# Kernel optimization log

Measured on AMD Instinct MI355X. Metric: run time of the kernel, lower is better.

The kernel has to match this reference:

```python
import jax, jax.numpy as jnp
import numpy as np

B, N, VDIM = 64, 256, 2048
LRDIM, EMBED = 64, 1024


def setup_inputs() -> dict:
    key = jax.random.key(0)
    ks = jax.random.split(key, 12)
    s = 1.0 / np.sqrt(VDIM)
    return {
        "Vmat": jax.random.normal(ks[0], (B, N, VDIM), dtype=jnp.float32),
        # weight-normed linear_U1: W = g * v / ||v||_row, bias b
        "U1_v": jax.random.normal(ks[1], (LRDIM, VDIM), dtype=jnp.float32) * s,
        "U1_g": jax.random.uniform(ks[2], (LRDIM,), dtype=jnp.float32, minval=0.5, maxval=1.5),
        "U1_b": jax.random.normal(ks[3], (LRDIM,), dtype=jnp.float32) * s,
        "U2_v": jax.random.normal(ks[4], (LRDIM, VDIM), dtype=jnp.float32) * s,
        "U2_g": jax.random.uniform(ks[5], (LRDIM,), dtype=jnp.float32, minval=0.5, maxval=1.5),
        "U2_b": jax.random.normal(ks[6], (LRDIM,), dtype=jnp.float32) * s,
        # final projection + BatchNorm1d affine params
        "W_lin": jax.random.normal(ks[7], (EMBED, VDIM), dtype=jnp.float32) * s,
        "b_lin": jax.random.normal(ks[8], (EMBED,), dtype=jnp.float32) * s,
        "bn_gamma": jnp.ones((EMBED,), dtype=jnp.float32),
        "bn_beta": jnp.zeros((EMBED,), dtype=jnp.float32),
    }


def _weight_norm(v, g):
    # torch weight_norm with dim=0: per output row
    return v * (g / jnp.linalg.norm(v, axis=1))[:, None]


def reference(Vmat, U1_v, U1_g, U1_b, U2_v, U2_g, U2_b, W_lin, b_lin, bn_gamma, bn_beta):
    # forward(Vmat, t_method='uncorr', model_num=6) -> UnCorrVmat_Detail path
    W1 = _weight_norm(U1_v, U1_g)
    W2 = _weight_norm(U2_v, U2_g)
    right = jax.nn.relu(jnp.einsum('bnv,kv->bnk', Vmat, W1) + U1_b)   # [B,N,LR]
    left = jax.nn.relu(jnp.einsum('bnv,kv->bnk', Vmat, W2) + U2_b)    # [B,N,LR]
    uncorr = jnp.einsum('bnk,bmk->bnm', left, right)                   # [B,N,N]
    # vectorized per-batch diag rsqrt normalization
    d = jax.lax.rsqrt(jnp.einsum('bii->bi', uncorr) + 1e-6)            # [B,N]
    uncorr = d[:, None, :] * uncorr * d[:, :, None]
    uncorr = 1.0 + jnp.eye(Vmat.shape[1], dtype=Vmat.dtype) - uncorr
    feats = jnp.mean(jnp.einsum('bnm,bmv->bnv', uncorr, Vmat), axis=1)  # [B,VDIM]
    # linear + BatchNorm1d (training mode: biased batch stats)
    x = feats @ W_lin.T + b_lin                                        # [B,EMBED]
    mu = jnp.mean(x, axis=0)
    var = jnp.mean(jnp.square(x - mu), axis=0)
    return bn_gamma * (x - mu) * jax.lax.rsqrt(var + 1e-5) + bn_beta
```

## Files before the change

### kernel.cpp

```cpp
#include <hip/hip_runtime.h>

#define B_ 64
#define N_ 256
#define V_ 2048
#define E_ 1024
#define MROWS 16384

typedef __bf16 bf16_t;
typedef bf16_t bf16x8 __attribute__((ext_vector_type(8)));
typedef float f32x4 __attribute__((ext_vector_type(4)));

#define OFF_S   0
#define OFF_LR  16384
#define OFF_FT  2113536
#define FTSZ    131072
#define OFF_WB  2637824

__device__ __forceinline__ void gload_lds16(const bf16_t* g, bf16_t* l) {
    __builtin_amdgcn_global_load_lds((const __attribute__((address_space(1))) void*)g,
                                     (__attribute__((address_space(3))) void*)l, 16, 0, 0);
}

__global__ void kprep(const float* __restrict__ U1v, const float* __restrict__ U1g,
                      const float* __restrict__ U2v, const float* __restrict__ U2g,
                      bf16_t* __restrict__ Wb) {
    __shared__ float red[256];
    __shared__ float sc;
    const int r = blockIdx.x;
    const float* v = (r < 64) ? (U1v + (size_t)r * V_) : (U2v + (size_t)(r - 64) * V_);
    float ss = 0.f;
    for (int i = threadIdx.x; i < V_; i += 256) { float x = v[i]; ss += x * x; }
    red[threadIdx.x] = ss;
    __syncthreads();
    for (int o = 128; o > 0; o >>= 1) {
        if (threadIdx.x < (unsigned)o) red[threadIdx.x] += red[threadIdx.x + o];
        __syncthreads();
    }
    if (threadIdx.x == 0) {
        float g = (r < 64) ? U1g[r] : U2g[r - 64];
        sc = g * rsqrtf(red[0]);
    }
    __syncthreads();
    const float s = sc;
    const int k = threadIdx.x * 8;
    float4 f0 = *(const float4*)(v + k);
    float4 f1 = *(const float4*)(v + k + 4);
    bf16x8 o;
    o[0] = (bf16_t)(f0.x * s); o[1] = (bf16_t)(f0.y * s);
    o[2] = (bf16_t)(f0.z * s); o[3] = (bf16_t)(f0.w * s);
    o[4] = (bf16_t)(f1.x * s); o[5] = (bf16_t)(f1.y * s);
    o[6] = (bf16_t)(f1.z * s); o[7] = (bf16_t)(f1.w * s);
    *(bf16x8*)(Wb + (size_t)r * V_ + k) = o;
}

#define BK 128
__global__ __launch_bounds__(256) void gemm_lr(
    const float* __restrict__ V, const bf16_t* __restrict__ Wb,
    const float* __restrict__ U1b, const float* __restrict__ U2b,
    float* __restrict__ LR) {
    __shared__ bf16_t As[32 * BK];
    __shared__ bf16_t Bs[128 * BK];
    const int t = threadIdx.x;
    const int m0 = blockIdx.x * 32;
    const int wv = t >> 6, lane = t & 63;
    const int lm = lane & 15, lq = lane >> 4;
    const int n0w = wv * 32;

    const int ar = t >> 3, au = t & 7;
    const float* aptr = V + (size_t)(m0 + ar) * V_ + au * 8;
    bf16_t* adst0 = &As[ar * BK + ((au ^ (ar & 15)) * 8)];
    bf16_t* adst1 = &As[ar * BK + (((au + 8) ^ (ar & 15)) * 8)];

    const int rloc = lane >> 4, cc = lane & 15;
    const int r15 = wv * 4 + rloc;
    const bf16_t* bgsrc = Wb + (size_t)r15 * V_ + (cc ^ r15) * 8;

    f32x4 acc[2][2];
#pragma unroll
    for (int i = 0; i < 2; ++i)
#pragma unroll
        for (int j = 0; j < 2; ++j) acc[i][j] = (f32x4){0.f, 0.f, 0.f, 0.f};

#pragma unroll
    for (int q = 0; q < 8; ++q)
        gload_lds16(bgsrc + (size_t)q * 16 * V_, &Bs[(q * 16 + wv * 4) * BK]);
    float4 ap0 = *(const float4*)(aptr);
    float4 ap1 = *(const float4*)(aptr + 4);
    float4 ap2 = *(const float4*)(aptr + 64);
    float4 ap3 = *(const float4*)(aptr + 68);

    for (int k0 = 0; k0 < V_; k0 += BK) {
        bf16x8 av0, av1;
        av0[0] = (bf16_t)ap0.x; av0[1] = (bf16_t)ap0.y; av0[2] = (bf16_t)ap0.z; av0[3] = (bf16_t)ap0.w;
        av0[4] = (bf16_t)ap1.x; av0[5] = (bf16_t)ap1.y; av0[6] = (bf16_t)ap1.z; av0[7] = (bf16_t)ap1.w;
        av1[0] = (bf16_t)ap2.x; av1[1] = (bf16_t)ap2.y; av1[2] = (bf16_t)ap2.z; av1[3] = (bf16_t)ap2.w;
        av1[4] = (bf16_t)ap3.x; av1[5] = (bf16_t)ap3.y; av1[6] = (bf16_t)ap3.z; av1[7] = (bf16_t)ap3.w;
        *(bf16x8*)adst0 = av0;
        *(bf16x8*)adst1 = av1;
        __syncthreads();

#pragma unroll
        for (int h = 0; h < 2; ++h) {
            bf16x8 af[2][2], bfr[2][2];
#pragma unroll
            for (int i = 0; i < 2; ++i)
#pragma unroll
                for (int kf = 0; kf < 2; ++kf)
                    af[i][kf] = *(bf16x8*)&As[(i * 16 + lm) * BK + ((((h * 2 + kf) * 4 + lq) ^ lm) * 8)];
#pragma unroll
            for (int j = 0; j < 2; ++j)
#pragma unroll
                for (int kf = 0; kf < 2; ++kf)
                    bfr[j][kf] = *(bf16x8*)&Bs[(n0w + j * 16 + lm) * BK + ((((h * 2 + kf) * 4 + lq) ^ lm) * 8)];
            if (h == 1 && k0 + BK < V_) {
                ap0 = *(const float4*)(aptr + k0 + BK);
                ap1 = *(const float4*)(aptr + k0 + BK + 4);
                ap2 = *(const float4*)(aptr + k0 + BK + 64);
                ap3 = *(const float4*)(aptr + k0 + BK + 68);
            }
#pragma unroll
            for (int i = 0; i < 2; ++i)
#pragma unroll
                for (int j = 0; j < 2; ++j) {
                    acc[i][j] = __builtin_amdgcn_mfma_f32_16x16x32_bf16(af[i][0], bfr[j][0], acc[i][j], 0, 0, 0);
                    acc[i][j] = __builtin_amdgcn_mfma_f32_16x16x32_bf16(af[i][1], bfr[j][1], acc[i][j], 0, 0, 0);
                }
        }
        __syncthreads();
        if (k0 + BK < V_) {
#pragma unroll
            for (int q = 0; q < 8; ++q)
                gload_lds16(bgsrc + (size_t)q * 16 * V_ + (k0 + BK), &Bs[(q * 16 + wv * 4) * BK]);
        }
    }
#pragma unroll
    for (int j = 0; j < 2; ++j) {
        const int n = n0w + j * 16 + lm;
        const float bi = (n < 64) ? U1b[n] : U2b[n - 64];
#pragma unroll
        for (int i = 0; i < 2; ++i)
#pragma unroll
            for (int r = 0; r < 4; ++r) {
                const int m = m0 + i * 16 + lq * 4 + r;
                LR[(size_t)m * 128 + n] = fmaxf(acc[i][j][r] + bi, 0.f);
            }
    }
}

__global__ __launch_bounds__(256) void kds(const float* __restrict__ LR, float* __restrict__ s) {
    __shared__ float dl[256];
    __shared__ float red[4][64];
    __shared__ float lbar[64];
    const int b = blockIdx.x, t = threadIdx.x;
    const float* Lb = LR + (size_t)b * N_ * 128;
    const float* row = Lb + (size_t)t * 128;
    float dd = 0.f;
#pragma unroll
    for (int k = 0; k < 64; k += 4) {
        float4 l = *(const float4*)(row + k);
        float4 r = *(const float4*)(row + 64 + k);
        dd += l.x * r.x + l.y * r.y + l.z * r.z + l.w * r.w;
    }
    const float dv = rsqrtf(dd + 1e-6f);
    dl[t] = dv;
    __syncthreads();
    const int k = t & 63, g = t >> 6;
    float acc = 0.f;
    for (int n = g; n < N_; n += 4)
        acc += dl[n] * Lb[(size_t)n * 128 + 64 + k];
    red[g][k] = acc;
    __syncthreads();
    if (t < 64) lbar[t] = red[0][t] + red[1][t] + red[2][t] + red[3][t];
    __syncthreads();
    float a2 = 0.f;
#pragma unroll 8
    for (int kk = 0; kk < 64; ++kk) a2 += lbar[kk] * row[kk];
    s[b * N_ + t] = ((float)(N_ + 1) - dv * a2) * (1.0f / (float)N_);
}

__global__ __launch_bounds__(256) void kfeats(const float* __restrict__ Vmat,
                                              const float* __restrict__ s,
                                              float* __restrict__ ftp) {
    const int b = blockIdx.x >> 3, vc = (blockIdx.x >> 2) & 1, mc = blockIdx.x & 3;
    __shared__ float sl[64];
    const int t = threadIdx.x;
    if (t < 64) sl[t] = s[b * N_ + mc * 64 + t];
    __syncthreads();
    const int v = vc * 1024 + t * 4;
    const float* base = Vmat + (size_t)b * N_ * V_ + (size_t)mc * 64 * V_ + v;
    float4 a = {0.f, 0.f, 0.f, 0.f};
    for (int m = 0; m < 64; m += 16) {
        float4 x[16];
#pragma unroll
        for (int u = 0; u < 16; ++u) x[u] = *(const float4*)(base + (size_t)(m + u) * V_);
#pragma unroll
        for (int u = 0; u < 16; ++u) {
            float sv = sl[m + u];
            a.x += sv * x[u].x; a.y += sv * x[u].y;
            a.z += sv * x[u].z; a.w += sv * x[u].w;
        }
    }
    float* dst = ftp + (size_t)mc * FTSZ;
    dst[(size_t)(v + 0) * 64 + b] = a.x;
    dst[(size_t)(v + 1) * 64 + b] = a.y;
    dst[(size_t)(v + 2) * 64 + b] = a.z;
    dst[(size_t)(v + 3) * 64 + b] = a.w;
}

__global__ __launch_bounds__(512) void klinbn(const float* __restrict__ ftp,
                                              const float* __restrict__ Wl,
                                              const float* __restrict__ gamma,
                                              const float* __restrict__ beta,
                                              float* __restrict__ out) {
    __shared__ float red[8][4][64];
    const int e0 = blockIdx.x * 4;
    const int t = threadIdx.x, b = t & 63, g = t >> 6;
    const float* w0 = Wl + (size_t)(e0 + 0) * V_ + g * 256;
    const float* w1 = Wl + (size_t)(e0 + 1) * V_ + g * 256;
    const float* w2 = Wl + (size_t)(e0 + 2) * V_ + g * 256;
    const float* w3 = Wl + (size_t)(e0 + 3) * V_ + g * 256;
    const float* f0 = ftp + 0 * FTSZ + (size_t)g * 256 * 64 + b;
    const float* f1 = ftp + 1 * FTSZ + (size_t)g * 256 * 64 + b;
    const float* f2 = ftp + 2 * FTSZ + (size_t)g * 256 * 64 + b;
    const float* f3 = ftp + 3 * FTSZ + (size_t)g * 256 * 64 + b;
    float a0 = 0.f, a1 = 0.f, a2 = 0.f, a3 = 0.f;
#pragma unroll 4
    for (int k = 0; k < 256; ++k) {
        const size_t o = (size_t)k * 64;
        float fv = (f0[o] + f1[o]) + (f2[o] + f3[o]);
        a0 += fv * w0[k]; a1 += fv * w1[k]; a2 += fv * w2[k]; a3 += fv * w3[k];
    }
    red[g][0][b] = a0; red[g][1][b] = a1; red[g][2][b] = a2; red[g][3][b] = a3;
    __syncthreads();
    if (t < 256) {
        const int e = t >> 6;
        float v = 0.f;
#pragma unroll
        for (int gg = 0; gg < 8; ++gg) v += red[gg][e][b];
        float sum = v;
#pragma unroll
        for (int o = 1; o < 64; o <<= 1) sum += __shfl_xor(sum, o, 64);
        float mu = sum * (1.f / 64.f);
        float dvv = v - mu;
        float q = dvv * dvv;
#pragma unroll
        for (int o = 1; o < 64; o <<= 1) q += __shfl_xor(q, o, 64);
        float inv = rsqrtf(q * (1.f / 64.f) + 1e-5f);
        red[0][e][b] = gamma[e0 + e] * dvv * inv + beta[e0 + e];
    }
    __syncthreads();
    if (t < 256) {
        const int b2 = t >> 2, j = t & 3;
        out[(size_t)b2 * E_ + e0 + j] = red[0][j][b2];
    }
}

extern "C" void kernel_launch(void* const* d_in, const int* in_sizes, int n_in,
                              void* d_out, int out_size, void* d_ws, size_t ws_size,
                              hipStream_t stream) {
    const float* Vmat = (const float*)d_in[0];
    const float* U1v  = (const float*)d_in[1];
    const float* U1g  = (const float*)d_in[2];
    const float* U1b  = (const float*)d_in[3];
    const float* U2v  = (const float*)d_in[4];
    const float* U2g  = (const float*)d_in[5];
    const float* U2b  = (const float*)d_in[6];
    const float* Wl   = (const float*)d_in[7];
    const float* gam  = (const float*)d_in[9];
    const float* bet  = (const float*)d_in[10];

    float*  ws     = (float*)d_ws;
    float*  s      = ws + OFF_S;
    float*  LR     = ws + OFF_LR;
    float*  ftp    = ws + OFF_FT;
    bf16_t* Wb     = (bf16_t*)(ws + OFF_WB);

    kprep  <<<128, 256, 0, stream>>>(U1v, U1g, U2v, U2g, Wb);
    gemm_lr<<<MROWS / 32, 256, 0, stream>>>(Vmat, Wb, U1b, U2b, LR);
    kds    <<<B_, 256, 0, stream>>>(LR, s);
    kfeats <<<B_ * 8, 256, 0, stream>>>(Vmat, s, ftp);
    klinbn <<<E_ / 4, 512, 0, stream>>>(ftp, Wl, gam, bet, (float*)d_out);
}
```

Baseline: 290.1 us.

## Fuse diagonal-scale kernel into feature reduction and drop partial-sum buffers

Merges the kernel that computes per-row scale factors with the weighted Vmat reduction. Each of 256 blocks now recomputes the scale vector for its batch and reduces all 256 rows for a 512-column slice, combining two row halves in shared memory. This removes one launch, the intermediate scale buffer, and the four partial feature copies the linear+BN kernel had to sum. The trade-off is that the LR-based scale computation is repeated four times per batch, and there are fewer, longer blocks (256 instead of 512) streaming Vmat.

```diff
diff --git a/kernel.cpp b/kernel.cpp
--- a/kernel.cpp
+++ b/kernel.cpp
@@ -10,7 +10,6 @@
 typedef bf16_t bf16x8 __attribute__((ext_vector_type(8)));
 typedef float f32x4 __attribute__((ext_vector_type(4)));
 
-#define OFF_S   0
 #define OFF_LR  16384
 #define OFF_FT  2113536
 #define FTSZ    131072
@@ -147,12 +146,17 @@
     }
 }
 
-__global__ __launch_bounds__(256) void kds(const float* __restrict__ LR, float* __restrict__ s) {
+__global__ __launch_bounds__(256) void kfs(const float* __restrict__ LR,
+                                           const float* __restrict__ Vmat,
+                                           float* __restrict__ F) {
+    const int b = blockIdx.x >> 2, vc = blockIdx.x & 3;
+    const float* Lb = LR + (size_t)b * N_ * 128;
     __shared__ float dl[256];
     __shared__ float red[4][64];
     __shared__ float lbar[64];
-    const int b = blockIdx.x, t = threadIdx.x;
-    const float* Lb = LR + (size_t)b * N_ * 128;
+    __shared__ float sl[256];
+    __shared__ float4 part[256];
+    const int t = threadIdx.x;
     const float* row = Lb + (size_t)t * 128;
     float dd = 0.f;
 #pragma unroll
@@ -175,39 +179,37 @@
     float a2 = 0.f;
 #pragma unroll 8
     for (int kk = 0; kk < 64; ++kk) a2 += lbar[kk] * row[kk];
-    s[b * N_ + t] = ((float)(N_ + 1) - dv * a2) * (1.0f / (float)N_);
-}
-
-__global__ __launch_bounds__(256) void kfeats(const float* __restrict__ Vmat,
-                                              const float* __restrict__ s,
-                                              float* __restrict__ ftp) {
-    const int b = blockIdx.x >> 3, vc = (blockIdx.x >> 2) & 1, mc = blockIdx.x & 3;
-    __shared__ float sl[64];
-    const int t = threadIdx.x;
-    if (t < 64) sl[t] = s[b * N_ + mc * 64 + t];
-    __syncthreads();
-    const int v = vc * 1024 + t * 4;
-    const float* base = Vmat + (size_t)b * N_ * V_ + (size_t)mc * 64 * V_ + v;
+    sl[t] = ((float)(N_ + 1) - dv * a2) * (1.0f / (float)N_);
+    __syncthreads();
+    const int v4 = t & 127, mh = t >> 7;
+    const int v = vc * 512 + v4 * 4;
+    const float* base = Vmat + (size_t)b * N_ * V_ + (size_t)mh * 128 * V_ + v;
     float4 a = {0.f, 0.f, 0.f, 0.f};
-    for (int m = 0; m < 64; m += 16) {
+    for (int m = 0; m < 128; m += 16) {
         float4 x[16];
 #pragma unroll
         for (int u = 0; u < 16; ++u) x[u] = *(const float4*)(base + (size_t)(m + u) * V_);
 #pragma unroll
         for (int u = 0; u < 16; ++u) {
-            float sv = sl[m + u];
+            float sv = sl[mh * 128 + m + u];
             a.x += sv * x[u].x; a.y += sv * x[u].y;
             a.z += sv * x[u].z; a.w += sv * x[u].w;
         }
     }
-    float* dst = ftp + (size_t)mc * FTSZ;
-    dst[(size_t)(v + 0) * 64 + b] = a.x;
-    dst[(size_t)(v + 1) * 64 + b] = a.y;
-    dst[(size_t)(v + 2) * 64 + b] = a.z;
-    dst[(size_t)(v + 3) * 64 + b] = a.w;
-}
-
-__global__ __launch_bounds__(512) void klinbn(const float* __restrict__ ftp,
+    part[t] = a;
+    __syncthreads();
+    if (mh == 0) {
+        float4 p = part[t + 128];
+        a = part[t];
+        a.x += p.x; a.y += p.y; a.z += p.z; a.w += p.w;
+        F[(size_t)(v + 0) * 64 + b] = a.x;
+        F[(size_t)(v + 1) * 64 + b] = a.y;
+        F[(size_t)(v + 2) * 64 + b] = a.z;
+        F[(size_t)(v + 3) * 64 + b] = a.w;
+    }
+}
+
+__global__ __launch_bounds__(512) void klinbn(const float* __restrict__ F,
                                               const float* __restrict__ Wl,
                                               const float* __restrict__ gamma,
                                               const float* __restrict__ beta,
@@ -219,15 +221,11 @@
     const float* w1 = Wl + (size_t)(e0 + 1) * V_ + g * 256;
     const float* w2 = Wl + (size_t)(e0 + 2) * V_ + g * 256;
     const float* w3 = Wl + (size_t)(e0 + 3) * V_ + g * 256;
-    const float* f0 = ftp + 0 * FTSZ + (size_t)g * 256 * 64 + b;
-    const float* f1 = ftp + 1 * FTSZ + (size_t)g * 256 * 64 + b;
-    const float* f2 = ftp + 2 * FTSZ + (size_t)g * 256 * 64 + b;
-    const float* f3 = ftp + 3 * FTSZ + (size_t)g * 256 * 64 + b;
+    const float* f0 = F + (size_t)g * 256 * 64 + b;
     float a0 = 0.f, a1 = 0.f, a2 = 0.f, a3 = 0.f;
 #pragma unroll 4
     for (int k = 0; k < 256; ++k) {
-        const size_t o = (size_t)k * 64;
-        float fv = (f0[o] + f1[o]) + (f2[o] + f3[o]);
+        float fv = f0[(size_t)k * 64];
         a0 += fv * w0[k]; a1 += fv * w1[k]; a2 += fv * w2[k]; a3 += fv * w3[k];
     }
     red[g][0][b] = a0; red[g][1][b] = a1; red[g][2][b] = a2; red[g][3][b] = a3;
@@ -270,14 +268,12 @@
     const float* bet  = (const float*)d_in[10];
 
     float*  ws     = (float*)d_ws;
-    float*  s      = ws + OFF_S;
     float*  LR     = ws + OFF_LR;
-    float*  ftp    = ws + OFF_FT;
+    float*  F      = ws + OFF_FT;
     bf16_t* Wb     = (bf16_t*)(ws + OFF_WB);
 
     kprep  <<<128, 256, 0, stream>>>(U1v, U1g, U2v, U2g, Wb);
     gemm_lr<<<MROWS / 32, 256, 0, stream>>>(Vmat, Wb, U1b, U2b, LR);
-    kds    <<<B_, 256, 0, stream>>>(LR, s);
-    kfeats <<<B_ * 8, 256, 0, stream>>>(Vmat, s, ftp);
-    klinbn <<<E_ / 4, 512, 0, stream>>>(ftp, Wl, gam, bet, (float*)d_out);
-}
+    kfs    <<<B_ * 4, 256, 0, stream>>>(LR, Vmat, F);
+    klinbn <<<E_ / 4, 512, 0, stream>>>(F, Wl, gam, bet, (float*)d_out);
+}
```

Result: faster. 280.1 us (-3.4%).
